# Optimization experiments

Hardware: AMD Instinct MI355X
Metric: run time of the kernel (lower is better)

## Reference

```python
import jax, jax.numpy as jnp
import numpy as np

B, S, D, H, DK, DV, DO = 2, 2048, 1024, 16, 64, 64, 1024


def setup_inputs() -> dict:
    key = jax.random.key(0)
    k0, k1, k2, k3, k4 = jax.random.split(key, 5)
    x = jax.random.normal(k0, (B, S, D), dtype=jnp.float32)
    # Stacked per-head projection weights (original uses H separate Linear(bias=False));
    # stored as [H, D, d_head] so q = x @ Wq[h] per head.
    Wq = jax.random.normal(k1, (H, D, DK), dtype=jnp.float32) * 0.02
    Wk = jax.random.normal(k2, (H, D, DK), dtype=jnp.float32) * 0.02
    Wv = jax.random.normal(k3, (H, D, DV), dtype=jnp.float32) * 0.02
    # Output projection Linear(dim_v*num_heads, dim_out, bias=False), stored [H*DV, DO]
    Wo = jax.random.normal(k4, (H * DV, DO), dtype=jnp.float32) * 0.02
    return {"x": x, "Wq": Wq, "Wk": Wk, "Wv": Wv, "Wo": Wo}


def reference(x, Wq, Wk, Wv, Wo):
    # Cross-head batched version of the per-head Python loop (same math).
    q = jnp.einsum('bsd,hde->bhse', x, Wq)  # [B,H,S,DK]
    k = jnp.einsum('bsd,hde->bhse', x, Wk)  # [B,H,S,DK]
    v = jnp.einsum('bsd,hde->bhse', x, Wv)  # [B,H,S,DV]
    scale = 1.0 / jnp.sqrt(jnp.asarray(k.shape[-1], dtype=x.dtype))
    scores = jnp.einsum('bhqe,bhke->bhqk', q, k) * scale  # [B,H,S,S]
    attn = jax.nn.softmax(scores, axis=-1)
    o = jnp.einsum('bhqk,bhke->bhqe', attn, v)  # [B,H,S,DV]
    # concat heads along feature dim (head order preserved)
    o = jnp.transpose(o, (0, 2, 1, 3)).reshape(o.shape[0], o.shape[2], -1)  # [B,S,H*DV]
    return o @ Wo  # [B,S,DO]
```

## Files before the change

kernel.cpp:

```cpp
#include <hip/hip_runtime.h>

typedef __bf16 bf16;
typedef __attribute__((ext_vector_type(8))) short short8;
typedef __attribute__((ext_vector_type(4))) short short4v;
typedef __attribute__((ext_vector_type(4))) float floatx4;

#define DEVINL __device__ __forceinline__

DEVINL void gll16(const void* g, void* l) {
  __builtin_amdgcn_global_load_lds((const __attribute__((address_space(1))) void*)g,
                                   (__attribute__((address_space(3))) void*)l, 16, 0, 0);
}

DEVINL float fast_exp2(float x) { return __builtin_amdgcn_exp2f(x); }

#define QSCALE 0.18033688011112042f

__global__ __launch_bounds__(256) void prep_all(const float* __restrict__ x,
                                                const float* __restrict__ Wq,
                                                const float* __restrict__ Wk,
                                                const float* __restrict__ Wv,
                                                const float* __restrict__ Wo,
                                                bf16* __restrict__ x_bf,
                                                bf16* __restrict__ WbigT,
                                                bf16* __restrict__ WoT) {
  __shared__ float tile[64][65];
  int bid = blockIdx.x;
  if (bid < 2048) {
    int i = (bid * 256 + threadIdx.x) * 8;
    float4 a = *(const float4*)(x + i);
    float4 b = *(const float4*)(x + i + 4);
    union { bf16 h[8]; short8 s; } u;
    u.h[0] = (bf16)a.x; u.h[1] = (bf16)a.y; u.h[2] = (bf16)a.z; u.h[3] = (bf16)a.w;
    u.h[4] = (bf16)b.x; u.h[5] = (bf16)b.y; u.h[6] = (bf16)b.z; u.h[7] = (bf16)b.w;
    *(short8*)(x_bf + i) = u.s;
    return;
  }
  int t = bid - 2048;
  int which = t >> 8;
  t &= 255;
  const float* in;
  bf16* out;
  int C, tilesC, tilesPerBatch;
  long inStride;
  if (which < 3) {
    in = which == 0 ? Wq : (which == 1 ? Wk : Wv);
    out = WbigT + (long)which * 1024 * 1024;
    C = 64; tilesC = 1; tilesPerBatch = 16; inStride = 65536;
  } else {
    in = Wo; out = WoT;
    C = 1024; tilesC = 16; tilesPerBatch = 256; inStride = 0;
  }
  int batch = t / tilesPerBatch;
  int tt = t % tilesPerBatch;
  int ri = tt / tilesC, ci = tt % tilesC;
  const float* src = in + batch * inStride;
  bf16* dst = out + batch * (long)65536 * (which < 3 ? 1 : 0);
  int tx = threadIdx.x & 63, ty = threadIdx.x >> 6;
#pragma unroll
  for (int i = 0; i < 16; i++) {
    int r = ty + i * 4;
    tile[r][tx] = src[(long)(ri * 64 + r) * C + ci * 64 + tx];
  }
  __syncthreads();
#pragma unroll
  for (int i = 0; i < 16; i++) {
    int c = ty + i * 4;
    dst[(long)(ci * 64 + c) * 1024 + ri * 64 + tx] = (bf16)tile[tx][c];
  }
}

template <int MODE>
__global__ __launch_bounds__(256) void gemm_bt(const bf16* __restrict__ A,
                                               const bf16* __restrict__ BT,
                                               float* __restrict__ Cout,
                                               int M, int N, int gridN,
                                               bf16* __restrict__ q_ws,
                                               bf16* __restrict__ k_ws,
                                               bf16* __restrict__ v_ws) {
  int cpx = gridDim.x >> 3;
  int swz = (blockIdx.x & 7) * cpx + (blockIdx.x >> 3);
  int bm = swz / gridN, bn = swz % gridN;
  __shared__ char lds[32768];
  char* ldsA = lds;
  char* ldsB = lds + 16384;
  int tid = threadIdx.x;
  int lane = tid & 63, wid = tid >> 6;
  int wr = wid >> 1, wc = wid & 1;
  floatx4 acc[4][4] = {};
  const long ldAB = 2048;
  const char* Abase = (const char*)A + (long)bm * 128 * ldAB;
  const char* Bbase = (const char*)BT + (long)bn * 128 * ldAB;

  for (int kt = 0; kt < 16; kt++) {
#pragma unroll
    for (int q = 0; q < 4; q++) {
      int r = q * 32 + (tid >> 3);
      int cb = ((tid & 7) * 16) ^ ((r & 7) << 4);
      gll16(Abase + (long)r * ldAB + kt * 128 + cb, ldsA + q * 4096 + wid * 1024);
      gll16(Bbase + (long)r * ldAB + kt * 128 + cb, ldsB + q * 4096 + wid * 1024);
    }
    asm volatile("s_waitcnt vmcnt(0)" ::: "memory");
    __syncthreads();
#pragma unroll
    for (int kk = 0; kk < 2; kk++) {
      short8 a[4], b[4];
#pragma unroll
      for (int mi = 0; mi < 4; mi++) {
        int row = wr * 64 + mi * 16 + (lane & 15);
        int col = (kk * 64 + (lane >> 4) * 16) ^ ((row & 7) << 4);
        a[mi] = *(const short8*)(ldsA + row * 128 + col);
      }
#pragma unroll
      for (int ni = 0; ni < 4; ni++) {
        int row = wc * 64 + ni * 16 + (lane & 15);
        int col = (kk * 64 + (lane >> 4) * 16) ^ ((row & 7) << 4);
        b[ni] = *(const short8*)(ldsB + row * 128 + col);
      }
#pragma unroll
      for (int mi = 0; mi < 4; mi++)
#pragma unroll
        for (int ni = 0; ni < 4; ni++)
          acc[mi][ni] = __builtin_amdgcn_mfma_f32_16x16x32_bf16(a[mi], b[ni], acc[mi][ni], 0, 0, 0);
    }
    __syncthreads();
  }

  if (MODE == 0 && bn >= 16) {
#pragma unroll
    for (int mi = 0; mi < 4; mi++)
#pragma unroll
      for (int ni = 0; ni < 4; ni++) {
        int local_c = wc * 64 + ni * 16 + (lane & 15);
        int ls0 = wr * 64 + mi * 16 + (lane >> 4) * 4;
        int sp = (ls0 & 64) | (ls0 & 32) | ((ls0 & 12) << 1) | ((ls0 & 16) >> 2);
        union { bf16 hh[4]; short4v s4; } u;
#pragma unroll
        for (int i = 0; i < 4; i++) u.hh[i] = (bf16)acc[mi][ni][i];
        *(short4v*)(lds + local_c * 256 + ((sp * 2) ^ ((local_c & 7) << 4))) = u.s4;
      }
    __syncthreads();
    int bb = bm >> 4;
    long sbase = (long)(bm & 15) * 128;
#pragma unroll
    for (int j = 0; j < 8; j++) {
      int local_c = wid * 32 + j * 4 + (lane >> 4);
      int chunk = lane & 15;
      int cg = bn * 128 + local_c;
      int h = (cg >> 6) & 15, e = cg & 63;
      long bh = (long)bb * 16 + h;
      char* dst = (char*)v_ws + ((bh * 64 + e) * 2048 + sbase) * 2 + chunk * 16;
      *(short8*)dst = *(const short8*)(lds + local_c * 256 + ((chunk * 16) ^ ((local_c & 7) << 4)));
    }
    return;
  }

#pragma unroll
  for (int mi = 0; mi < 4; mi++)
#pragma unroll
    for (int ni = 0; ni < 4; ni++)
#pragma unroll
      for (int i = 0; i < 4; i++) {
        float v = acc[mi][ni][i];
        int r = bm * 128 + wr * 64 + mi * 16 + (lane >> 4) * 4 + i;
        int c = bn * 128 + wc * 64 + ni * 16 + (lane & 15);
        if (MODE == 0) {
          int b = r >> 11, s = r & 2047;
          int which = c >> 10, h = (c >> 6) & 15, e = c & 63;
          long bh = b * 16 + h;
          if (which == 0) q_ws[(bh * 2048 + s) * 64 + e] = (bf16)(v * QSCALE);
          else            k_ws[(bh * 2048 + s) * 64 + e] = (bf16)v;
        } else {
          Cout[(long)r * N + c] = v;
        }
      }
}

__global__ __launch_bounds__(512, 2) void attn_kernel(const bf16* __restrict__ q_ws,
                                                      const bf16* __restrict__ k_ws,
                                                      const bf16* __restrict__ v_ws,
                                                      bf16* __restrict__ obuf) {
  int wgid = ((blockIdx.x & 7) << 5) + (blockIdx.x >> 3);
  int qt = wgid & 7;
  int bh = wgid >> 3;
  int b = bh >> 4, h = bh & 15;
  __shared__ char lds[65536];
  char* kbuf = lds;
  char* vbuf = lds + 32768;
  int tid = threadIdx.x, lane = tid & 63, wid = tid >> 6;
  int ql = lane & 15, g = lane >> 4;

  const char* kbase = (const char*)k_ws + (long)bh * 2048 * 128;
  const char* vbase = (const char*)v_ws + (long)bh * 64 * 4096;

  int srow = wid * 8 + (lane >> 3);
  int scb = ((lane & 7) * 16) ^ (((lane >> 3) & 7) << 4);

#define STAGE(t_) do {                                                              \
    gll16(kbase + ((long)(t_) * 64 + srow) * 128 + scb,                             \
          kbuf + ((t_) & 3) * 8192 + wid * 1024);                                   \
    gll16(vbase + (long)srow * 4096 + (long)(t_) * 128 + scb,                       \
          vbuf + ((t_) & 3) * 8192 + wid * 1024);                                   \
  } while (0)

#define WAIT2_BAR do {                                                              \
    asm volatile("s_waitcnt vmcnt(2)" ::: "memory");                                \
    __builtin_amdgcn_s_barrier();                                                   \
    asm volatile("" ::: "memory");                                                  \
  } while (0)

  int sw = (ql & 7) << 4;
  int fof0 = ql * 128 + ((g * 16) ^ sw);
  int fof1 = ql * 128 + ((64 + g * 16) ^ sw);

  const bf16* qrowL = q_ws + ((long)bh * 2048 + qt * 256 + wid * 32 + ql) * 64 + 8 * g;
  short8 qL0 = *(const short8*)(qrowL);
  short8 qL1 = *(const short8*)(qrowL + 32);
  short8 qH0 = *(const short8*)(qrowL + 1024);
  short8 qH1 = *(const short8*)(qrowL + 1024 + 32);

  union { bf16 hh[8]; short8 s; } uo1;
#pragma unroll
  for (int i = 0; i < 8; i++) uo1.hh[i] = (bf16)1.0f;
  const short8 ones = uo1.s;

  floatx4 lL = {}, lH = {};
  floatx4 oL[4] = {}, oH[4] = {};
  floatx4 saL[4], saH[4];
  short8 pbL[2], pbH[2];

#define QKSTEP(kc) do {                                                             \
    __builtin_amdgcn_s_setprio(1);                                                  \
    _Pragma("unroll") for (int t_ = 0; t_ < 4; t_++) {                              \
      short8 kf = *(const short8*)((kc) + fof0 + t_ * 2048);                        \
      saL[t_] = __builtin_amdgcn_mfma_f32_16x16x32_bf16(kf, qL0, (floatx4){}, 0, 0, 0); \
      saH[t_] = __builtin_amdgcn_mfma_f32_16x16x32_bf16(kf, qH0, (floatx4){}, 0, 0, 0); \
    }                                                                               \
    _Pragma("unroll") for (int t_ = 0; t_ < 4; t_++) {                              \
      short8 kf = *(const short8*)((kc) + fof1 + t_ * 2048);                        \
      saL[t_] = __builtin_amdgcn_mfma_f32_16x16x32_bf16(kf, qL1, saL[t_], 0, 0, 0); \
      saH[t_] = __builtin_amdgcn_mfma_f32_16x16x32_bf16(kf, qH1, saH[t_], 0, 0, 0); \
    }                                                                               \
    __builtin_amdgcn_s_setprio(0);                                                  \
  } while (0)

#define SM_HALF(sa, pb, l_acc, o_acc) do {                                          \
    if (__builtin_expect(l_acc[0] > 1e30f, 0)) {                                    \
      const float c_ = 7.8886091e-31f;                                  \
      _Pragma("unroll") for (int t_ = 0; t_ < 4; t_++)                              \
        _Pragma("unroll") for (int i_ = 0; i_ < 4; i_++) o_acc[t_][i_] *= c_;       \
      _Pragma("unroll") for (int i_ = 0; i_ < 4; i_++) l_acc[i_] *= c_;             \
    }                                                                               \
    _Pragma("unroll") for (int kk_ = 0; kk_ < 2; kk_++) {                           \
      union { bf16 hh[8]; short8 s; } up_;                                          \
      _Pragma("unroll") for (int r_ = 0; r_ < 4; r_++)                              \
        up_.hh[r_] = (bf16)fast_exp2(sa[2 * kk_][r_]);                              \
      _Pragma("unroll") for (int r_ = 0; r_ < 4; r_++)                              \
        up_.hh[4 + r_] = (bf16)fast_exp2(sa[2 * kk_ + 1][r_]);                      \
      pb[kk_] = up_.s;                                                              \
    }                                                                               \
  } while (0)

#define SMSTEP do { SM_HALF(saL, pbL, lL, oL); SM_HALF(saH, pbH, lH, oH); } while (0)

#define PVSTEP(vc) do {                                                             \
    __builtin_amdgcn_s_setprio(1);                                                  \
    lL = __builtin_amdgcn_mfma_f32_16x16x32_bf16(ones, pbL[0], lL, 0, 0, 0);        \
    lL = __builtin_amdgcn_mfma_f32_16x16x32_bf16(ones, pbL[1], lL, 0, 0, 0);        \
    lH = __builtin_amdgcn_mfma_f32_16x16x32_bf16(ones, pbH[0], lH, 0, 0, 0);        \
    lH = __builtin_amdgcn_mfma_f32_16x16x32_bf16(ones, pbH[1], lH, 0, 0, 0);        \
    _Pragma("unroll") for (int t_ = 0; t_ < 4; t_++) {                              \
      short8 vf = *(const short8*)((vc) + fof0 + t_ * 2048);                        \
      oL[t_] = __builtin_amdgcn_mfma_f32_16x16x32_bf16(vf, pbL[0], oL[t_], 0, 0, 0);\
      oH[t_] = __builtin_amdgcn_mfma_f32_16x16x32_bf16(vf, pbH[0], oH[t_], 0, 0, 0);\
    }                                                                               \
    _Pragma("unroll") for (int t_ = 0; t_ < 4; t_++) {                              \
      short8 vf = *(const short8*)((vc) + fof1 + t_ * 2048);                        \
      oL[t_] = __builtin_amdgcn_mfma_f32_16x16x32_bf16(vf, pbL[1], oL[t_], 0, 0, 0);\
      oH[t_] = __builtin_amdgcn_mfma_f32_16x16x32_bf16(vf, pbH[1], oH[t_], 0, 0, 0);\
    }                                                                               \
    __builtin_amdgcn_s_setprio(0);                                                  \
  } while (0)

  STAGE(0); STAGE(1);
  WAIT2_BAR;
  QKSTEP(kbuf + 0 * 8192);
  STAGE(2);
  SMSTEP;
  WAIT2_BAR;
  STAGE(3);
  QKSTEP(kbuf + 1 * 8192);

  for (int t = 1; t <= 29; t++) {
    PVSTEP(vbuf + ((t - 1) & 3) * 8192);
    SMSTEP;
    WAIT2_BAR;
    if (t <= 28) STAGE(t + 3);
    QKSTEP(kbuf + ((t + 1) & 3) * 8192);
  }

  PVSTEP(vbuf + (29 & 3) * 8192);
  SMSTEP;
  __syncthreads();
  QKSTEP(kbuf + (31 & 3) * 8192);

  PVSTEP(vbuf + (30 & 3) * 8192);
  SMSTEP;
  PVSTEP(vbuf + (31 & 3) * 8192);

#undef STAGE
#undef WAIT2_BAR
#undef QKSTEP
#undef SM_HALF
#undef SMSTEP
#undef PVSTEP

  {
    float invL = 1.f / lL[0];
    float invH = 1.f / lH[0];
    int s = qt * 256 + wid * 32 + ql;
    bf16* orowL = obuf + ((long)b * 2048 + s) * 1024 + h * 64;
    bf16* orowH = orowL + 16 * 1024;
#pragma unroll
    for (int t = 0; t < 4; t++) {
      union { bf16 hh[4]; short4v s4; } uo;
#pragma unroll
      for (int r = 0; r < 4; r++) uo.hh[r] = (bf16)(oL[t][r] * invL);
      *(short4v*)(orowL + t * 16 + 4 * g) = uo.s4;
#pragma unroll
      for (int r = 0; r < 4; r++) uo.hh[r] = (bf16)(oH[t][r] * invH);
      *(short4v*)(orowH + t * 16 + 4 * g) = uo.s4;
    }
  }
}

extern "C" void kernel_launch(void* const* d_in, const int* in_sizes, int n_in,
                              void* d_out, int out_size, void* d_ws, size_t ws_size,
                              hipStream_t stream) {
  const float* x  = (const float*)d_in[0];
  const float* Wq = (const float*)d_in[1];
  const float* Wk = (const float*)d_in[2];
  const float* Wv = (const float*)d_in[3];
  const float* Wo = (const float*)d_in[4];
  float* out = (float*)d_out;

  char* ws = (char*)d_ws;
  bf16* x_bf  = (bf16*)(ws);
  bf16* WbigT = (bf16*)(ws + 8388608);
  bf16* WoT   = (bf16*)(ws + 14680064);
  bf16* q_ws  = (bf16*)(ws + 16777216);
  bf16* k_ws  = (bf16*)(ws + 25165824);
  bf16* v_ws  = (bf16*)(ws + 33554432);
  bf16* obuf  = (bf16*)(ws + 41943040);

  prep_all<<<3072, 256, 0, stream>>>(x, Wq, Wk, Wv, Wo, x_bf, WbigT, WoT);
  gemm_bt<0><<<32 * 24, 256, 0, stream>>>(x_bf, WbigT, nullptr, 4096, 3072, 24, q_ws, k_ws, v_ws);
  attn_kernel<<<256, 512, 0, stream>>>(q_ws, k_ws, v_ws, obuf);
  gemm_bt<1><<<32 * 8, 256, 0, stream>>>(obuf, WoT, out, 4096, 1024, 8, nullptr, nullptr, nullptr);
}
```

Baseline: 116.3 us.

## Replace QKV projection GEMM with 256x256-tile double-buffered pipelined kernel

The QKV projection moves from the generic 128x128 gemm_bt to a dedicated 256x256-tile kernel with 512 threads and 128KB of dynamic LDS. It double-buffers global-to-LDS loads and interleaves them with MFMA phases using explicit waitcnt, barriers and setprio. The aim is more data reuse per tile and load latency hidden behind compute. The grid drops to 192 workgroups on a 256-CU part, which can leave CUs idle and unbalanced. The output GEMM becomes its own non-templated kernel.

```diff
diff --git a/kernel.cpp b/kernel.cpp
--- a/kernel.cpp
+++ b/kernel.cpp
@@ -70,14 +70,150 @@
   }
 }
 
-template <int MODE>
-__global__ __launch_bounds__(256) void gemm_bt(const bf16* __restrict__ A,
-                                               const bf16* __restrict__ BT,
-                                               float* __restrict__ Cout,
-                                               int M, int N, int gridN,
-                                               bf16* __restrict__ q_ws,
-                                               bf16* __restrict__ k_ws,
-                                               bf16* __restrict__ v_ws) {
+__global__ __launch_bounds__(512, 2) void gemm256_qkv(const bf16* __restrict__ A,
+                                                      const bf16* __restrict__ BT,
+                                                      bf16* __restrict__ q_ws,
+                                                      bf16* __restrict__ k_ws,
+                                                      bf16* __restrict__ v_ws) {
+  extern __shared__ char lds[];
+  int swz = (blockIdx.x & 7) * 24 + (blockIdx.x >> 3);
+  int bm = swz / 12, bn = swz % 12;
+  int tid = threadIdx.x, lane = tid & 63, wid = tid >> 6;
+  int wm = wid >> 2, wn = wid & 3;
+  int ql = lane & 15, g = lane >> 4;
+  int sw = (ql & 7) << 4;
+  int hB = wn >> 1;
+  char* ldsA = lds;
+  char* ldsB = lds + 65536;
+
+  const char* Abase = (const char*)A + (long)bm * 256 * 2048;
+  const char* Bbase = (const char*)BT + (long)bn * 256 * 2048;
+  int scb = ((tid & 7) * 16) ^ (((tid >> 3) & 7) << 4);
+
+  floatx4 acc[8][4] = {};
+  short8 aF[4], bF[4];
+
+#define STG(dst0, src0, kt_, h_) do {                                              \
+    _Pragma("unroll") for (int j_ = 0; j_ < 2; j_++)                               \
+      gll16((src0) + (long)((h_) * 128 + j_ * 64 + (tid >> 3)) * 2048              \
+                   + (kt_) * 128 + scb,                                            \
+            (dst0) + ((kt_) & 1) * 32768 + (h_) * 16384 + j_ * 8192 + wid * 1024); \
+  } while (0)
+#define LDA(slot_, frh_, kk_) do {                                                 \
+    _Pragma("unroll") for (int j_ = 0; j_ < 4; j_++)                               \
+      aF[j_] = *(const short8*)(ldsA + (slot_) * 32768 + wm * 16384 +              \
+               (((frh_) * 4 + j_) * 16 + ql) * 128 + (((kk_) * 64 + g * 16) ^ sw));\
+  } while (0)
+#define LDB(slot_, kk_) do {                                                       \
+    _Pragma("unroll") for (int f_ = 0; f_ < 4; f_++)                               \
+      bF[f_] = *(const short8*)(ldsB + (slot_) * 32768 + hB * 16384 +              \
+               ((wn & 1) * 64 + f_ * 16 + ql) * 128 + (((kk_) * 64 + g * 16) ^ sw));\
+  } while (0)
+#define MFMA16(frh_) do {                                                          \
+    __builtin_amdgcn_s_setprio(1);                                                 \
+    _Pragma("unroll") for (int j_ = 0; j_ < 4; j_++)                               \
+      _Pragma("unroll") for (int f_ = 0; f_ < 4; f_++)                             \
+        acc[(frh_) * 4 + j_][f_] = __builtin_amdgcn_mfma_f32_16x16x32_bf16(        \
+            aF[j_], bF[f_], acc[(frh_) * 4 + j_][f_], 0, 0, 0);                    \
+    __builtin_amdgcn_s_setprio(0);                                                 \
+  } while (0)
+#define BAR __builtin_amdgcn_s_barrier()
+#define LG0 asm volatile("s_waitcnt lgkmcnt(0)" ::: "memory")
+
+  STG(ldsB, Bbase, 0, 0); STG(ldsB, Bbase, 0, 1);
+  STG(ldsA, Abase, 0, 0); STG(ldsA, Abase, 0, 1);
+  STG(ldsB, Bbase, 1, 0);
+
+  for (int it = 0; it < 8; it++) {
+    int b1 = 2 * it + 1, a2 = 2 * it + 2, b2 = 2 * it + 3;
+    bool more = it < 7;
+    asm volatile("s_waitcnt vmcnt(2)" ::: "memory");
+    BAR;
+    LDA(0, 0, 0); LDB(0, 0);
+    STG(ldsA, Abase, b1, 0);
+    BAR; LG0; MFMA16(0); BAR;
+    LDA(0, 1, 0);
+    STG(ldsA, Abase, b1, 1);
+    BAR; LG0; MFMA16(1); BAR;
+    LDA(0, 0, 1); LDB(0, 1);
+    STG(ldsB, Bbase, b1, 1);
+    BAR; LG0; MFMA16(0); BAR;
+    LDA(0, 1, 1);
+    if (more) STG(ldsB, Bbase, a2, 0);
+    BAR; LG0; MFMA16(1); BAR;
+    if (more) { asm volatile("s_waitcnt vmcnt(2)" ::: "memory"); }
+    else      { asm volatile("s_waitcnt vmcnt(0)" ::: "memory"); }
+    BAR;
+    LDA(1, 0, 0); LDB(1, 0);
+    if (more) STG(ldsB, Bbase, a2, 1);
+    BAR; LG0; MFMA16(0); BAR;
+    LDA(1, 1, 0);
+    if (more) STG(ldsA, Abase, a2, 0);
+    BAR; LG0; MFMA16(1); BAR;
+    LDA(1, 0, 1); LDB(1, 1);
+    if (more) STG(ldsA, Abase, a2, 1);
+    BAR; LG0; MFMA16(0); BAR;
+    LDA(1, 1, 1);
+    if (more) STG(ldsB, Bbase, b2, 0);
+    BAR; LG0; MFMA16(1); BAR;
+  }
+#undef STG
+#undef LDA
+#undef LDB
+#undef MFMA16
+#undef BAR
+#undef LG0
+
+  if (bn < 8) {
+    bf16* dst = (bn < 4) ? q_ws : k_ws;
+    float scale = (bn < 4) ? QSCALE : 1.0f;
+#pragma unroll
+    for (int fr = 0; fr < 8; fr++)
+#pragma unroll
+      for (int fc = 0; fc < 4; fc++)
+#pragma unroll
+        for (int i = 0; i < 4; i++) {
+          int r = bm * 256 + wm * 128 + fr * 16 + g * 4 + i;
+          int c = bn * 256 + wn * 64 + fc * 16 + ql;
+          int b = r >> 11, s = r & 2047;
+          int h = (c >> 6) & 15, e = c & 63;
+          long bh = (long)b * 16 + h;
+          dst[(bh * 2048 + s) * 64 + e] = (bf16)(acc[fr][fc][i] * scale);
+        }
+  } else {
+#pragma unroll
+    for (int fr = 0; fr < 8; fr++)
+#pragma unroll
+      for (int fc = 0; fc < 4; fc++) {
+        int local_c = wn * 64 + fc * 16 + ql;
+        int ls0 = wm * 128 + fr * 16 + g * 4;
+        int s6 = ls0 & 63;
+        int sp = (ls0 & ~63) | (s6 & 35) | ((s6 & 12) << 1) | ((s6 & 16) >> 2);
+        union { bf16 hh[4]; short4v s4; } u;
+#pragma unroll
+        for (int i = 0; i < 4; i++) u.hh[i] = (bf16)acc[fr][fc][i];
+        *(short4v*)(lds + local_c * 512 + ((sp * 2) ^ ((local_c & 7) << 4))) = u.s4;
+      }
+    __syncthreads();
+    int b = bm >> 3;
+    long sbase = (long)(bm & 7) * 256;
+#pragma unroll
+    for (int j = 0; j < 16; j++) {
+      int local_c = wid * 32 + j * 2 + (lane >> 5);
+      int chunk = lane & 31;
+      int cg = bn * 256 + local_c;
+      int h = (cg >> 6) & 15, e = cg & 63;
+      long bh = (long)b * 16 + h;
+      char* dstp = (char*)v_ws + ((bh * 64 + e) * 2048 + sbase) * 2 + chunk * 16;
+      *(short8*)dstp = *(const short8*)(lds + local_c * 512 + ((chunk * 16) ^ ((local_c & 7) << 4)));
+    }
+  }
+}
+
+__global__ __launch_bounds__(256) void gemm_out(const bf16* __restrict__ A,
+                                                const bf16* __restrict__ BT,
+                                                float* __restrict__ Cout,
+                                                int N, int gridN) {
   int cpx = gridDim.x >> 3;
   int swz = (blockIdx.x & 7) * cpx + (blockIdx.x >> 3);
   int bm = swz / gridN, bn = swz % gridN;
@@ -126,53 +262,15 @@
     __syncthreads();
   }
 
-  if (MODE == 0 && bn >= 16) {
-#pragma unroll
-    for (int mi = 0; mi < 4; mi++)
-#pragma unroll
-      for (int ni = 0; ni < 4; ni++) {
-        int local_c = wc * 64 + ni * 16 + (lane & 15);
-        int ls0 = wr * 64 + mi * 16 + (lane >> 4) * 4;
-        int sp = (ls0 & 64) | (ls0 & 32) | ((ls0 & 12) << 1) | ((ls0 & 16) >> 2);
-        union { bf16 hh[4]; short4v s4; } u;
-#pragma unroll
-        for (int i = 0; i < 4; i++) u.hh[i] = (bf16)acc[mi][ni][i];
-        *(short4v*)(lds + local_c * 256 + ((sp * 2) ^ ((local_c & 7) << 4))) = u.s4;
-      }
-    __syncthreads();
-    int bb = bm >> 4;
-    long sbase = (long)(bm & 15) * 128;
-#pragma unroll
-    for (int j = 0; j < 8; j++) {
-      int local_c = wid * 32 + j * 4 + (lane >> 4);
-      int chunk = lane & 15;
-      int cg = bn * 128 + local_c;
-      int h = (cg >> 6) & 15, e = cg & 63;
-      long bh = (long)bb * 16 + h;
-      char* dst = (char*)v_ws + ((bh * 64 + e) * 2048 + sbase) * 2 + chunk * 16;
-      *(short8*)dst = *(const short8*)(lds + local_c * 256 + ((chunk * 16) ^ ((local_c & 7) << 4)));
-    }
-    return;
-  }
-
 #pragma unroll
   for (int mi = 0; mi < 4; mi++)
 #pragma unroll
     for (int ni = 0; ni < 4; ni++)
 #pragma unroll
       for (int i = 0; i < 4; i++) {
-        float v = acc[mi][ni][i];
         int r = bm * 128 + wr * 64 + mi * 16 + (lane >> 4) * 4 + i;
         int c = bn * 128 + wc * 64 + ni * 16 + (lane & 15);
-        if (MODE == 0) {
-          int b = r >> 11, s = r & 2047;
-          int which = c >> 10, h = (c >> 6) & 15, e = c & 63;
-          long bh = b * 16 + h;
-          if (which == 0) q_ws[(bh * 2048 + s) * 64 + e] = (bf16)(v * QSCALE);
-          else            k_ws[(bh * 2048 + s) * 64 + e] = (bf16)v;
-        } else {
-          Cout[(long)r * N + c] = v;
-        }
+        Cout[(long)r * N + c] = acc[mi][ni][i];
       }
 }
 
@@ -353,8 +451,11 @@
   bf16* v_ws  = (bf16*)(ws + 33554432);
   bf16* obuf  = (bf16*)(ws + 41943040);
 
+  hipFuncSetAttribute((const void*)gemm256_qkv,
+                      hipFuncAttributeMaxDynamicSharedMemorySize, 131072);
+
   prep_all<<<3072, 256, 0, stream>>>(x, Wq, Wk, Wv, Wo, x_bf, WbigT, WoT);
-  gemm_bt<0><<<32 * 24, 256, 0, stream>>>(x_bf, WbigT, nullptr, 4096, 3072, 24, q_ws, k_ws, v_ws);
+  gemm256_qkv<<<192, 512, 131072, stream>>>(x_bf, WbigT, q_ws, k_ws, v_ws);
   attn_kernel<<<256, 512, 0, stream>>>(q_ws, k_ws, v_ws, obuf);
-  gemm_bt<1><<<32 * 8, 256, 0, stream>>>(obuf, WoT, out, 4096, 1024, 8, nullptr, nullptr, nullptr);
-}
+  gemm_out<<<256, 256, 0, stream>>>(obuf, WoT, out, 1024, 8);
+}
```

Result: faster. 102.9 us (-11.5%).
